# Optimization experiments

Measured on AMD Instinct MI355X. Metric: run time of the kernel, lower is better.

## Reference

```python
import jax, jax.numpy as jnp
import numpy as np

EPS = 1e-7  # K.epsilon()

_LC = np.zeros((3, 3, 3), np.float32)  # Levi-Civita for 1x1->1
_LC[0, 1, 2] = _LC[1, 2, 0] = _LC[2, 0, 1] = 1.0
_LC[0, 2, 1] = _LC[2, 1, 0] = _LC[1, 0, 2] = -1.0


def _ssp(x):
    # shifted softplus: log(0.5*exp(x)+0.5)
    return jnp.log(0.5 * jnp.exp(x) + 0.5)


def _radial(image, w1, b1, w2, b2):
    # Sequential([Dense(32), Dense(feat)]) -- linear Dense layers (no activation)
    return (image @ w1 + b1) @ w2 + b2  # (m, a, b, feat)


def setup_inputs() -> dict:
    key = jax.random.key(0)
    ks = jax.random.split(key, 16)
    M, A, RBF, F, SI, H = 4, 256, 64, 32, 32, 32
    inp = {}
    inp["image"] = jax.random.uniform(ks[0], (M, A, A, RBF), dtype=jnp.float32)
    inp["vectors"] = jax.random.normal(ks[1], (M, A, A, 3), dtype=jnp.float32)
    inp["feat0"] = jax.random.normal(ks[2], (M, A, F, 1), dtype=jnp.float32)
    inp["feat1"] = jax.random.normal(ks[3], (M, A, F, 3), dtype=jnp.float32)
    i = 4
    for rin in (0, 1):
        for fro in (0, 1):
            tag = f"{rin}{fro}"
            inp[f"w1_{tag}"] = jax.random.normal(ks[i], (RBF, H)) / np.sqrt(RBF).astype(np.float32)
            inp[f"b1_{tag}"] = jnp.zeros((H,), jnp.float32)
            i += 1
            inp[f"w2_{tag}"] = jax.random.normal(ks[i], (H, F)) / np.sqrt(np.float32(H))
            inp[f"b2_{tag}"] = jnp.zeros((F,), jnp.float32)
            i += 1
    inp["w_si0"] = jax.random.normal(ks[i], (SI, 2 * F)) / np.sqrt(np.float32(2 * F)); i += 1
    inp["w_si1"] = jax.random.normal(ks[i], (SI, 3 * F)) / np.sqrt(np.float32(3 * F)); i += 1
    inp["b_act0"] = jnp.zeros((SI,), jnp.float32)
    inp["b_act1"] = jnp.zeros((SI,), jnp.float32)
    return inp


def reference(image, vectors, feat0, feat1,
              w1_00, b1_00, w2_00, b2_00,
              w1_01, b1_01, w2_01, b2_01,
              w1_10, b1_10, w2_10, b2_10,
              w1_11, b1_11, w2_11, b2_11,
              w_si0, w_si1, b_act0, b_act1):
    # mask where |r_ab| < eps (self-pairs / padding)
    mask = (jnp.sqrt(jnp.sum(vectors * vectors, axis=-1)) < EPS)[..., None]  # (m,a,b,1)

    def filt0(w1, b1, w2, b2):
        return _radial(image, w1, b1, w2, b2)  # (m,a,b,F), implicit rep index of size 1

    def filt1(w1, b1, w2, b2):
        r = jnp.where(mask, 0.0, _radial(image, w1, b1, w2, b2))  # masked radial
        return vectors[:, :, :, None, :] * r[..., None]  # (m,a,b,F,3)

    f0_in0 = filt0(w1_00, b1_00, w2_00, b2_00)
    f1_in0 = filt1(w1_01, b1_01, w2_01, b2_01)
    f0_in1 = filt0(w1_10, b1_10, w2_10, b2_10)
    f1_in1 = filt1(w1_11, b1_11, w2_11, b2_11)

    # point convolution (sum over neighbor atoms b)
    out_0x0_0 = jnp.einsum('mabf,mbfj->mafj', f0_in0, feat0)   # (m,a,F,1)
    out_0x1_1 = jnp.einsum('mabfi,mbfj->mafi', f1_in0, feat0)  # (m,a,F,3)
    out_1x0_1 = jnp.einsum('mabf,mbfj->mafj', f0_in1, feat1)   # (m,a,F,3)
    cg0 = jnp.eye(3, dtype=image.dtype)[None]                  # (1,3,3): 1x1->0
    out_1x1_0 = jnp.einsum('ijk,mabfj,mbfk->mafi', cg0, f1_in1, feat1)  # (m,a,F,1)
    lc = jnp.asarray(_LC, image.dtype)                         # 1x1->1
    out_1x1_1 = jnp.einsum('ijk,mabfj,mbfk->mafi', lc, f1_in1, feat1)   # (m,a,F,3)

    # concat along channel dim per output RO
    cat0 = jnp.concatenate([out_0x0_0, out_1x1_0], axis=2)  # (m,a,2F,1)
    cat1 = jnp.concatenate([out_0x1_1, out_1x0_1, out_1x1_1], axis=2)  # (m,a,3F,3)

    # self-interaction: einsum('mafi,gf->maig') then transpose -> (m,a,g,i)
    si0 = jnp.einsum('mafi,gf->magi', cat0, w_si0)  # (m,a,SI,1)
    si1 = jnp.einsum('mafi,gf->magi', cat1, w_si1)  # (m,a,SI,3)

    # equivariant activation
    o0 = _ssp(si0 + b_act0[None, None, :, None])
    n1 = jnp.sqrt(jnp.maximum(jnp.sum(si1 * si1, axis=-1), EPS))  # norm_with_epsilon
    a1 = _ssp(n1 + b_act1)
    o1 = si1 * (a1 / n1)[..., None]
    return (o0, o1)
```

## Files before the change

kernel.cpp:

```cpp
#include <hip/hip_runtime.h>
#include <math.h>

#define M_ 4
#define A_ 256
#define RBF_ 64
#define F_ 32
#define H_ 32
#define SI_ 32
#define TF_ 128

typedef __attribute__((ext_vector_type(8))) short bf16x8;
typedef __attribute__((ext_vector_type(4))) float f32x4;
typedef __attribute__((ext_vector_type(3))) float f32x3;

__device__ __forceinline__ unsigned short f2bf(float f) {
  union { float f; unsigned u; } v; v.f = f;
  unsigned r = v.u + 0x7FFFu + ((v.u >> 16) & 1u);
  return (unsigned short)(r >> 16);
}

__device__ __forceinline__ unsigned pack2bf(float lo, float hi) {
  union { float f; unsigned u; } a, b; a.f = lo; b.f = hi;
  return __builtin_amdgcn_perm(b.u + 0x8000u, a.u + 0x8000u, 0x07060302u);
}

__device__ __forceinline__ float sspf(float x) {
  return fmaxf(x, 0.f) + log1pf(expf(-fabsf(x))) - 0.6931471805599453f;
}

__global__ __launch_bounds__(256) void combine_weights(
    const float* __restrict__ w1_00, const float* __restrict__ b1_00,
    const float* __restrict__ w2_00, const float* __restrict__ b2_00,
    const float* __restrict__ w1_01, const float* __restrict__ b1_01,
    const float* __restrict__ w2_01, const float* __restrict__ b2_01,
    const float* __restrict__ w1_10, const float* __restrict__ b1_10,
    const float* __restrict__ w2_10, const float* __restrict__ b2_10,
    const float* __restrict__ w1_11, const float* __restrict__ b1_11,
    const float* __restrict__ w2_11, const float* __restrict__ b2_11,
    unsigned short* __restrict__ wsT, float* __restrict__ bcw)
{
  const float* w1s[4] = {w1_00, w1_01, w1_10, w1_11};
  const float* b1s[4] = {b1_00, b1_01, b1_10, b1_11};
  const float* w2s[4] = {w2_00, w2_01, w2_10, w2_11};
  const float* b2s[4] = {b2_00, b2_01, b2_10, b2_11};
  int tid = blockIdx.x * 256 + threadIdx.x;
  int k   = tid >> 7;
  int tf  = tid & 127;
  int tag = tf >> 5, f = tf & 31;
  const float* w1 = w1s[tag];
  const float* w2 = w2s[tag];
  float s = 0.f;
  for (int h = 0; h < H_; ++h) s += w1[k * H_ + h] * w2[h * F_ + f];
  wsT[tf * 64 + k] = f2bf(s);
  if (tid < TF_) {
    const float* b1 = b1s[tag];
    const float* b2 = b2s[tag];
    float sb = b2[f];
    for (int h = 0; h < H_; ++h) sb += b1[h] * w2[h * F_ + f];
    bcw[tf] = sb;
  }
}

__global__ __launch_bounds__(512, 4) void conv_fused(
    const float* __restrict__ image, const float* __restrict__ vectors,
    const float* __restrict__ feat0, const float* __restrict__ feat1,
    const unsigned short* __restrict__ wsT, const float* __restrict__ bcw,
    const float* __restrict__ w_si0, const float* __restrict__ w_si1,
    const float* __restrict__ b_act0, const float* __restrict__ b_act1,
    float* __restrict__ out)
{
  __shared__ __align__(16) unsigned short sA[256 * 72];
  __shared__ __align__(16) float sV[A_ * 3];
  float* const cat = sV;

  const int t    = threadIdx.x;
  const int ma   = blockIdx.x;
  const int m    = ma >> 8;
  const int l    = t & 63;
  const int n    = l & 15;
  const int quad = l >> 4;
  const int wu    = __builtin_amdgcn_readfirstlane(t >> 6);
  const int role  = (wu + ((ma & 3) << 1)) & 7;
  const int which = role & 1;
  const int tag   = role >> 1;
  const int ct    = tag * 2 + which;
  const int f     = which * 16 + n;

  const unsigned short* wr = wsT + (ct * 16 + n) * 64 + quad * 8;
  const bf16x8 w0 = *(const bf16x8*)(wr);
  const bf16x8 w1 = *(const bf16x8*)(wr + 32);
  const float  bc = bcw[ct * 16 + n];

  const int srow = t >> 2;
  const int sc16 = (t & 3) << 4;
  const float* g1 = image + (size_t)ma * (A_ * RBF_) + srow * RBF_ + sc16;
  const float* g2 = g1 + 128 * RBF_;
  unsigned short* w1p = &sA[srow * 72 + sc16];
  unsigned short* w2p = &sA[(srow + 128) * 72 + sc16];

  float4 a0 = *(const float4*)(g1);
  float4 a1 = *(const float4*)(g1 + 4);
  float4 a2 = *(const float4*)(g1 + 8);
  float4 a3 = *(const float4*)(g1 + 12);
  {
    const float* vsrc = vectors + (size_t)ma * (A_ * 3);
    sV[t] = vsrc[t];
    if (t < 256) sV[t + 512] = vsrc[t + 512];
  }
  {
    uint4 pk;
    pk.x = pack2bf(a0.x, a0.y); pk.y = pack2bf(a0.z, a0.w);
    pk.z = pack2bf(a1.x, a1.y); pk.w = pack2bf(a1.z, a1.w);
    *(uint4*)w1p = pk;
    pk.x = pack2bf(a2.x, a2.y); pk.y = pack2bf(a2.z, a2.w);
    pk.z = pack2bf(a3.x, a3.y); pk.w = pack2bf(a3.z, a3.w);
    *(uint4*)(w1p + 8) = pk;
  }
  float4 hb = *(const float4*)(g2);

  const int b0q = quad * 4;
  const float* p0c = feat0 + (size_t)(m * A_ + b0q) * F_ + f;
  const float* p1c = feat1 + ((size_t)(m * A_ + b0q) * F_ + f) * 3;
  const float* svc = &sV[b0q * 3];
  const unsigned short* aBc = &sA[n * 72 + quad * 8];

  float gx[2][4], gy[2][4], gz[2][4];
  float pA = 0.f, pB0 = 0.f, pB1 = 0.f, pB2 = 0.f;

#define PF(BUF) { \
    if (tag <= 1) { \
      _Pragma("unroll") \
      for (int r = 0; r < 4; ++r) gx[BUF][r] = p0c[r * F_]; \
    } else { \
      _Pragma("unroll") \
      for (int r = 0; r < 4; ++r) { \
        f32x3 v = *(const f32x3*)(p1c + r * (F_ * 3)); \
        gx[BUF][r] = v[0]; gy[BUF][r] = v[1]; gz[BUF][r] = v[2]; \
      } \
    } \
    p0c += 16 * F_; p1c += 16 * F_ * 3; }

#define BODY(AOFF, SOFF, GX, GY, GZ) { \
    const bf16x8 a0_ = *(const bf16x8*)(aBc + (AOFF)); \
    const bf16x8 a1_ = *(const bf16x8*)(aBc + (AOFF) + 32); \
    f32x4 v0, v1, v2; \
    if (tag & 1) { \
      v0 = *(const f32x4*)(svc + (SOFF)); \
      v1 = *(const f32x4*)(svc + (SOFF) + 4); \
      v2 = *(const f32x4*)(svc + (SOFF) + 8); \
    } \
    f32x4 acc = {bc, bc, bc, bc}; \
    acc = __builtin_amdgcn_mfma_f32_16x16x32_bf16(a0_, w0, acc, 0, 0, 0); \
    acc = __builtin_amdgcn_mfma_f32_16x16x32_bf16(a1_, w1, acc, 0, 0, 0); \
    if (tag == 0) {             \
      _Pragma("unroll") \
      for (int r = 0; r < 4; ++r) pA += acc[r] * GX[r]; \
    } else if (tag == 1) {      \
      float s; \
      s = acc[0] * GX[0]; \
      pB0 = fmaf(v0[0], s, pB0); pB1 = fmaf(v0[1], s, pB1); pB2 = fmaf(v0[2], s, pB2); \
      s = acc[1] * GX[1]; \
      pB0 = fmaf(v0[3], s, pB0); pB1 = fmaf(v1[0], s, pB1); pB2 = fmaf(v1[1], s, pB2); \
      s = acc[2] * GX[2]; \
      pB0 = fmaf(v1[2], s, pB0); pB1 = fmaf(v1[3], s, pB1); pB2 = fmaf(v2[0], s, pB2); \
      s = acc[3] * GX[3]; \
      pB0 = fmaf(v2[1], s, pB0); pB1 = fmaf(v2[2], s, pB1); pB2 = fmaf(v2[3], s, pB2); \
    } else if (tag == 2) {      \
      _Pragma("unroll") \
      for (int r = 0; r < 4; ++r) { \
        const float Rr = acc[r]; \
        pB0 += Rr * GX[r]; pB1 += Rr * GY[r]; pB2 += Rr * GZ[r]; \
      } \
    } else {                    \
      { const float Rr = acc[0], ax = GX[0], ay = GY[0], az = GZ[0]; \
        const float vx = v0[0], vy = v0[1], vz = v0[2]; \
        float d = vx * ax; d = fmaf(vy, ay, d); d = fmaf(vz, az, d); \
        pA = fmaf(Rr, d, pA); \
        float c0 = vy * az; c0 = fmaf(-vz, ay, c0); pB0 = fmaf(Rr, c0, pB0); \
        float c1 = vz * ax; c1 = fmaf(-vx, az, c1); pB1 = fmaf(Rr, c1, pB1); \
        float c2 = vx * ay; c2 = fmaf(-vy, ax, c2); pB2 = fmaf(Rr, c2, pB2); } \
      { const float Rr = acc[1], ax = GX[1], ay = GY[1], az = GZ[1]; \
        const float vx = v0[3], vy = v1[0], vz = v1[1]; \
        float d = vx * ax; d = fmaf(vy, ay, d); d = fmaf(vz, az, d); \
        pA = fmaf(Rr, d, pA); \
        float c0 = vy * az; c0 = fmaf(-vz, ay, c0); pB0 = fmaf(Rr, c0, pB0); \
        float c1 = vz * ax; c1 = fmaf(-vx, az, c1); pB1 = fmaf(Rr, c1, pB1); \
        float c2 = vx * ay; c2 = fmaf(-vy, ax, c2); pB2 = fmaf(Rr, c2, pB2); } \
      { const float Rr = acc[2], ax = GX[2], ay = GY[2], az = GZ[2]; \
        const float vx = v1[2], vy = v1[3], vz = v2[0]; \
        float d = vx * ax; d = fmaf(vy, ay, d); d = fmaf(vz, az, d); \
        pA = fmaf(Rr, d, pA); \
        float c0 = vy * az; c0 = fmaf(-vz, ay, c0); pB0 = fmaf(Rr, c0, pB0); \
        float c1 = vz * ax; c1 = fmaf(-vx, az, c1); pB1 = fmaf(Rr, c1, pB1); \
        float c2 = vx * ay; c2 = fmaf(-vy, ax, c2); pB2 = fmaf(Rr, c2, pB2); } \
      { const float Rr = acc[3], ax = GX[3], ay = GY[3], az = GZ[3]; \
        const float vx = v2[1], vy = v2[2], vz = v2[3]; \
        float d = vx * ax; d = fmaf(vy, ay, d); d = fmaf(vz, az, d); \
        pA = fmaf(Rr, d, pA); \
        float c0 = vy * az; c0 = fmaf(-vz, ay, c0); pB0 = fmaf(Rr, c0, pB0); \
        float c1 = vz * ax; c1 = fmaf(-vx, az, c1); pB1 = fmaf(Rr, c1, pB1); \
        float c2 = vx * ay; c2 = fmaf(-vy, ax, c2); pB2 = fmaf(Rr, c2, pB2); } \
    } }

#define H2PACK_R() { \
    uint2 pk; pk.x = pack2bf(hb.x, hb.y); pk.y = pack2bf(hb.z, hb.w); \
    *(uint2*)w2p = pk; w2p += 4; \
    g2 += 4; hb = *(const float4*)(g2); }
#define H2PACK_F() { \
    uint2 pk; pk.x = pack2bf(hb.x, hb.y); pk.y = pack2bf(hb.z, hb.w); \
    *(uint2*)w2p = pk; }

#define BARRIER() { \
    asm volatile("s_waitcnt lgkmcnt(0)" ::: "memory"); \
    __builtin_amdgcn_s_barrier(); \
    asm volatile("" ::: "memory"); }

  PF(0)
  BARRIER();

  #pragma unroll 1
  for (int d = 0; d < 4; ++d) {
    PF(1)
    BODY(0, 0, gx[0], gy[0], gz[0])
    PF(0)
    BODY(1152, 48, gx[1], gy[1], gz[1])
    aBc += 2304; svc += 96;
    { uint2 pk; pk.x = pack2bf(hb.x, hb.y); pk.y = pack2bf(hb.z, hb.w);
      *(uint2*)w2p = pk; }
    w2p += 4;
    if (d < 3) { g2 += 4; hb = *(const float4*)(g2); }
  }
  BARRIER();

  #pragma unroll 1
  for (int d = 0; d < 4; ++d) {
    PF(1)
    BODY(0, 0, gx[0], gy[0], gz[0])
    if (d < 3) PF(0)
    BODY(1152, 48, gx[1], gy[1], gz[1])
    aBc += 2304; svc += 96;
  }

#define QRED(x) { x += __shfl_xor(x, 16); x += __shfl_xor(x, 32); }
  QRED(pA) QRED(pB0) QRED(pB1) QRED(pB2)
  __syncthreads();
  if (quad == 0) {
    if (tag == 0) {
      cat[f] = pA;
    } else if (tag == 1) {
      cat[64 + f * 3 + 0] = pB0; cat[64 + f * 3 + 1] = pB1; cat[64 + f * 3 + 2] = pB2;
    } else if (tag == 2) {
      cat[160 + f * 3 + 0] = pB0; cat[160 + f * 3 + 1] = pB1; cat[160 + f * 3 + 2] = pB2;
    } else {
      cat[32 + f] = pA;
      cat[256 + f * 3 + 0] = pB0; cat[256 + f * 3 + 1] = pB1; cat[256 + f * 3 + 2] = pB2;
    }
  }
  __syncthreads();

  if (t < 256) {
    const int g = t >> 3, p = t & 7;
    const float* wrow = w_si1 + g * 96 + p * 12;
    const float* c1 = &cat[64 + p * 36];
    float s0 = 0.f, s1 = 0.f, s2 = 0.f;
    #pragma unroll
    for (int k = 0; k < 12; ++k) {
      const float wv = wrow[k];
      s0 = fmaf(c1[k * 3 + 0], wv, s0);
      s1 = fmaf(c1[k * 3 + 1], wv, s1);
      s2 = fmaf(c1[k * 3 + 2], wv, s2);
    }
    s0 += __shfl_xor(s0, 1); s0 += __shfl_xor(s0, 2); s0 += __shfl_xor(s0, 4);
    s1 += __shfl_xor(s1, 1); s1 += __shfl_xor(s1, 2); s1 += __shfl_xor(s1, 4);
    s2 += __shfl_xor(s2, 1); s2 += __shfl_xor(s2, 2); s2 += __shfl_xor(s2, 4);
    if (p == 0) {
      const float n2 = s0 * s0 + s1 * s1 + s2 * s2;
      const float n1 = sqrtf(fmaxf(n2, 1e-7f));
      const float a1 = sspf(n1 + b_act1[g]);
      const float sc = a1 / n1;
      const int ob = M_ * A_ * SI_ + (ma * SI_ + g) * 3;
      out[ob + 0] = s0 * sc; out[ob + 1] = s1 * sc; out[ob + 2] = s2 * sc;
    }
  } else if (t < 320) {
    const int t2 = t - 256, g = t2 >> 1, p = t2 & 1;
    const float* wrow = w_si0 + g * 64 + p * 32;
    const float* c0 = &cat[p * 32];
    float s = 0.f;
    #pragma unroll 8
    for (int k = 0; k < 32; ++k) s = fmaf(c0[k], wrow[k], s);
    s += __shfl_xor(s, 1);
    if (p == 0) out[ma * SI_ + g] = sspf(s + b_act0[g]);
  }
}

extern "C" void kernel_launch(void* const* d_in, const int* in_sizes, int n_in,
                              void* d_out, int out_size, void* d_ws, size_t ws_size,
                              hipStream_t stream) {
  const float* image   = (const float*)d_in[0];
  const float* vectors = (const float*)d_in[1];
  const float* feat0   = (const float*)d_in[2];
  const float* feat1   = (const float*)d_in[3];
  const float* w_si0   = (const float*)d_in[20];
  const float* w_si1   = (const float*)d_in[21];
  const float* b_act0  = (const float*)d_in[22];
  const float* b_act1  = (const float*)d_in[23];
  unsigned short* wsT = (unsigned short*)d_ws;
  float* bcw  = (float*)((char*)d_ws + 16384);
  float* out  = (float*)d_out;

  combine_weights<<<32, 256, 0, stream>>>(
      (const float*)d_in[4],  (const float*)d_in[5],
      (const float*)d_in[6],  (const float*)d_in[7],
      (const float*)d_in[8],  (const float*)d_in[9],
      (const float*)d_in[10], (const float*)d_in[11],
      (const float*)d_in[12], (const float*)d_in[13],
      (const float*)d_in[14], (const float*)d_in[15],
      (const float*)d_in[16], (const float*)d_in[17],
      (const float*)d_in[18], (const float*)d_in[19],
      wsT, bcw);

  conv_fused<<<M_ * A_, 512, 0, stream>>>(
      image, vectors, feat0, feat1, wsT, bcw,
      w_si0, w_si1, b_act0, b_act1, out);
}
```

Baseline: 156.3 us.

## Stream image tiles via global_load_lds into a triple-buffered fp32 LDS ring

Replaces the up-front load of the whole image row into LDS as bf16 with a direct global-to-LDS async copy (global_load_lds) of 32-row fp32 chunks into three rotating buffers, using an XOR swizzle. The bf16 packing moves to just before each MFMA, and a per-chunk barrier with vmcnt waits overlaps the next chunks' loads with compute. The goal is to hide image load latency and cut the register and VALU cost of staging. The price is a barrier per chunk, repeated conversion work, and fragile hand-counted vmcnt values that must match the outstanding loads, including the feature prefetches.

```diff
diff --git a/kernel.cpp b/kernel.cpp
--- a/kernel.cpp
+++ b/kernel.cpp
@@ -69,7 +69,7 @@
     const float* __restrict__ b_act0, const float* __restrict__ b_act1,
     float* __restrict__ out)
 {
-  __shared__ __align__(16) unsigned short sA[256 * 72];
+  __shared__ __align__(16) float sB[3][32 * 64];
   __shared__ __align__(16) float sV[A_ * 3];
   float* const cat = sV;
 
@@ -91,38 +91,31 @@
   const bf16x8 w1 = *(const bf16x8*)(wr + 32);
   const float  bc = bcw[ct * 16 + n];
 
-  const int srow = t >> 2;
-  const int sc16 = (t & 3) << 4;
-  const float* g1 = image + (size_t)ma * (A_ * RBF_) + srow * RBF_ + sc16;
-  const float* g2 = g1 + 128 * RBF_;
-  unsigned short* w1p = &sA[srow * 72 + sc16];
-  unsigned short* w2p = &sA[(srow + 128) * 72 + sc16];
-
-  float4 a0 = *(const float4*)(g1);
-  float4 a1 = *(const float4*)(g1 + 4);
-  float4 a2 = *(const float4*)(g1 + 8);
-  float4 a3 = *(const float4*)(g1 + 12);
+  const char* gBase = (const char*)image + (size_t)ma * (A_ * RBF_ * 4);
+  const int lrow = l >> 4;
+  const int gOffLane = (4 * wu + lrow) * 256 +
+                       (((l & 15) ^ ((4 * wu + lrow) & 7)) << 4);
+
+#define GLOAD(DST, C) { \
+    __builtin_amdgcn_global_load_lds( \
+      (const __attribute__((address_space(1))) void*)(gBase + (C) * 8192 + gOffLane), \
+      (__attribute__((address_space(3))) void*)((char*)(DST) + (wu << 10)), \
+      16, 0, 0); }
+
+  const int sw = n & 7;
+  const int b0 = n * 256 + (((2 * quad)     ^ sw) << 4);
+  const int b1 = n * 256 + (((2 * quad + 1) ^ sw) << 4);
+
   {
     const float* vsrc = vectors + (size_t)ma * (A_ * 3);
     sV[t] = vsrc[t];
     if (t < 256) sV[t + 512] = vsrc[t + 512];
   }
-  {
-    uint4 pk;
-    pk.x = pack2bf(a0.x, a0.y); pk.y = pack2bf(a0.z, a0.w);
-    pk.z = pack2bf(a1.x, a1.y); pk.w = pack2bf(a1.z, a1.w);
-    *(uint4*)w1p = pk;
-    pk.x = pack2bf(a2.x, a2.y); pk.y = pack2bf(a2.z, a2.w);
-    pk.z = pack2bf(a3.x, a3.y); pk.w = pack2bf(a3.z, a3.w);
-    *(uint4*)(w1p + 8) = pk;
-  }
-  float4 hb = *(const float4*)(g2);
 
   const int b0q = quad * 4;
   const float* p0c = feat0 + (size_t)(m * A_ + b0q) * F_ + f;
   const float* p1c = feat1 + ((size_t)(m * A_ + b0q) * F_ + f) * 3;
   const float* svc = &sV[b0q * 3];
-  const unsigned short* aBc = &sA[n * 72 + quad * 8];
 
   float gx[2][4], gy[2][4], gz[2][4];
   float pA = 0.f, pB0 = 0.f, pB1 = 0.f, pB2 = 0.f;
@@ -140,15 +133,25 @@
     } \
     p0c += 16 * F_; p1c += 16 * F_ * 3; }
 
-#define BODY(AOFF, SOFF, GX, GY, GZ) { \
-    const bf16x8 a0_ = *(const bf16x8*)(aBc + (AOFF)); \
-    const bf16x8 a1_ = *(const bf16x8*)(aBc + (AOFF) + 32); \
+#define BODYF(BUFP, TPAR, SOFF, GX, GY, GZ) { \
+    const char* _ab = (const char*)(BUFP) + (TPAR) * 4096; \
+    const f32x4 r0 = *(const f32x4*)(_ab + b0); \
+    const f32x4 r1 = *(const f32x4*)(_ab + b1); \
+    const f32x4 r2 = *(const f32x4*)(_ab + b0 + 128); \
+    const f32x4 r3 = *(const f32x4*)(_ab + b1 + 128); \
     f32x4 v0, v1, v2; \
     if (tag & 1) { \
       v0 = *(const f32x4*)(svc + (SOFF)); \
       v1 = *(const f32x4*)(svc + (SOFF) + 4); \
       v2 = *(const f32x4*)(svc + (SOFF) + 8); \
     } \
+    uint4 pk0, pk1; \
+    pk0.x = pack2bf(r0[0], r0[1]); pk0.y = pack2bf(r0[2], r0[3]); \
+    pk0.z = pack2bf(r1[0], r1[1]); pk0.w = pack2bf(r1[2], r1[3]); \
+    pk1.x = pack2bf(r2[0], r2[1]); pk1.y = pack2bf(r2[2], r2[3]); \
+    pk1.z = pack2bf(r3[0], r3[1]); pk1.w = pack2bf(r3[2], r3[3]); \
+    const bf16x8 a0_ = __builtin_bit_cast(bf16x8, pk0); \
+    const bf16x8 a1_ = __builtin_bit_cast(bf16x8, pk1); \
     f32x4 acc = {bc, bc, bc, bc}; \
     acc = __builtin_amdgcn_mfma_f32_16x16x32_bf16(a0_, w0, acc, 0, 0, 0); \
     acc = __builtin_amdgcn_mfma_f32_16x16x32_bf16(a1_, w1, acc, 0, 0, 0); \
@@ -202,43 +205,29 @@
         float c2 = vx * ay; c2 = fmaf(-vy, ax, c2); pB2 = fmaf(Rr, c2, pB2); } \
     } }
 
-#define H2PACK_R() { \
-    uint2 pk; pk.x = pack2bf(hb.x, hb.y); pk.y = pack2bf(hb.z, hb.w); \
-    *(uint2*)w2p = pk; w2p += 4; \
-    g2 += 4; hb = *(const float4*)(g2); }
-#define H2PACK_F() { \
-    uint2 pk; pk.x = pack2bf(hb.x, hb.y); pk.y = pack2bf(hb.z, hb.w); \
-    *(uint2*)w2p = pk; }
-
-#define BARRIER() { \
-    asm volatile("s_waitcnt lgkmcnt(0)" ::: "memory"); \
-    __builtin_amdgcn_s_barrier(); \
-    asm volatile("" ::: "memory"); }
-
+  float* cur = sB[0]; float* nxt = sB[1]; float* fut = sB[2];
+  GLOAD(cur, 0)
+  GLOAD(nxt, 1)
   PF(0)
-  BARRIER();
+  asm volatile("s_waitcnt vmcnt(5)" ::: "memory");
+  asm volatile("s_waitcnt lgkmcnt(0)" ::: "memory");
+  __builtin_amdgcn_s_barrier();
+  asm volatile("" ::: "memory");
 
   #pragma unroll 1
-  for (int d = 0; d < 4; ++d) {
+  for (int c = 0; c < 8; ++c) {
+    if (c < 6) GLOAD(fut, c + 2)
     PF(1)
-    BODY(0, 0, gx[0], gy[0], gz[0])
-    PF(0)
-    BODY(1152, 48, gx[1], gy[1], gz[1])
-    aBc += 2304; svc += 96;
-    { uint2 pk; pk.x = pack2bf(hb.x, hb.y); pk.y = pack2bf(hb.z, hb.w);
-      *(uint2*)w2p = pk; }
-    w2p += 4;
-    if (d < 3) { g2 += 4; hb = *(const float4*)(g2); }
-  }
-  BARRIER();
-
-  #pragma unroll 1
-  for (int d = 0; d < 4; ++d) {
-    PF(1)
-    BODY(0, 0, gx[0], gy[0], gz[0])
-    if (d < 3) PF(0)
-    BODY(1152, 48, gx[1], gy[1], gz[1])
-    aBc += 2304; svc += 96;
+    BODYF(cur, 0, 0, gx[0], gy[0], gz[0])
+    if (c < 7) PF(0)
+    BODYF(cur, 1, 48, gx[1], gy[1], gz[1])
+    svc += 96;
+    if (c < 7) {
+      asm volatile("s_waitcnt vmcnt(9)" ::: "memory");
+      __builtin_amdgcn_s_barrier();
+      asm volatile("" ::: "memory");
+      float* tmp = cur; cur = nxt; nxt = fut; fut = tmp;
+    }
   }
 
 #define QRED(x) { x += __shfl_xor(x, 16); x += __shfl_xor(x, 32); }
```

After: 166.9 us. 6.8% more time.
